# Kernel tuning notes

Hardware: AMD Instinct MI355X
Metric: run time of the kernel (lower is better)

## Reference

```python
import jax, jax.numpy as jnp
import numpy as np

HIDDEN = 64
INPUT = 19


def _lstm_layer(x, Wih, Whh, bih, bhh):
    # x: [B, T, I]; Wih: [4H, I]; Whh: [4H, H]; biases: [4H]
    B, T, _ = x.shape
    H = Whh.shape[1]
    # Input contribution for all timesteps at once (big GEMM).
    zx = jnp.einsum('bti,gi->btg', x, Wih) + bih + bhh  # [B, T, 4H]

    def step(carry, z_t):
        h, c = carry
        z = z_t + h @ Whh.T  # [B, 4H]
        i, f, g, o = jnp.split(z, 4, axis=-1)  # torch gate order: i, f, g, o
        i = jax.nn.sigmoid(i)
        f = jax.nn.sigmoid(f)
        g = jnp.tanh(g)
        o = jax.nn.sigmoid(o)
        c = f * c + i * g
        h = o * jnp.tanh(c)
        return (h, c), h

    h0 = jnp.zeros((B, H), x.dtype)
    (_, _), hs = jax.lax.scan(step, (h0, h0), jnp.swapaxes(zx, 0, 1))
    return jnp.swapaxes(hs, 0, 1)  # [B, T, H]


def setup_inputs() -> dict:
    key = jax.random.key(0)
    ks = jax.random.split(key, 12)
    B, T = 4096, 168
    s = 1.0 / np.sqrt(HIDDEN)  # torch LSTM/Linear init scale
    u = lambda k, shape: jax.random.uniform(k, shape, jnp.float32, -s, s)
    return {
        'x': jax.random.normal(ks[0], (B, T, INPUT), jnp.float32),
        'Wih0': u(ks[1], (4 * HIDDEN, INPUT)),
        'Whh0': u(ks[2], (4 * HIDDEN, HIDDEN)),
        'bih0': u(ks[3], (4 * HIDDEN,)),
        'bhh0': u(ks[4], (4 * HIDDEN,)),
        'Wih1': u(ks[5], (4 * HIDDEN, HIDDEN)),
        'Whh1': u(ks[6], (4 * HIDDEN, HIDDEN)),
        'bih1': u(ks[7], (4 * HIDDEN,)),
        'bhh1': u(ks[8], (4 * HIDDEN,)),
        'Wfc': u(ks[9], (1, HIDDEN)),
        'bfc': u(ks[10], (1,)),
    }


def reference(x, Wih0, Whh0, bih0, bhh0, Wih1, Whh1, bih1, bhh1, Wfc, bfc):
    h1 = _lstm_layer(x, Wih0, Whh0, bih0, bhh0)   # [B, T, H]
    h2 = _lstm_layer(h1, Wih1, Whh1, bih1, bhh1)  # [B, T, H]
    out = h2[:, -1, :] @ Wfc.T + bfc              # [B, 1]
    return out.squeeze(-1)                        # [B]
```

## Files before the change

kernel.cpp:

```cpp
#include <hip/hip_runtime.h>
#include <math.h>

#define T_STEPS 168
#define INP     19
#define HID     64
#define ROWS    16
#define NTH     512
#define HSTH    72
#define XSTH    40

typedef _Float16 half8   __attribute__((ext_vector_type(8)));
typedef float    floatx4 __attribute__((ext_vector_type(4)));

#define KSIG  (-1.4426950408889634f)
#define KTANH ( 2.8853900817779268f)

#if defined(__has_builtin)
#  if __has_builtin(__builtin_amdgcn_exp2f)
#    define EXP2(x) __builtin_amdgcn_exp2f(x)
#  else
#    define EXP2(x) exp2f(x)
#  endif
#else
#  define EXP2(x) exp2f(x)
#endif

__device__ __forceinline__ float sig_pre(float a) {
    return __builtin_amdgcn_rcpf(1.0f + EXP2(a));
}
__device__ __forceinline__ float tanh_pre(float a) {
    return 1.0f - 2.0f * __builtin_amdgcn_rcpf(1.0f + EXP2(a));
}

__global__ __launch_bounds__(NTH) __attribute__((amdgpu_waves_per_eu(2, 2)))
void lstm2_mfma6_kernel(const float* __restrict__ x,
                        const float* __restrict__ Wih0, const float* __restrict__ Whh0,
                        const float* __restrict__ bih0, const float* __restrict__ bhh0,
                        const float* __restrict__ Wih1, const float* __restrict__ Whh1,
                        const float* __restrict__ bih1, const float* __restrict__ bhh1,
                        const float* __restrict__ Wfc,  const float* __restrict__ bfc,
                        float* __restrict__ out)
{
    __shared__ __align__(16) _Float16 xf [2][ROWS][XSTH];
    __shared__ __align__(16) _Float16 h1f[2][ROWS][HSTH];
    __shared__ __align__(16) _Float16 h2f[2][ROWS][HSTH];
    __shared__ float hout[ROWS][HID];

    const int tid  = threadIdx.x;
    const int b0   = blockIdx.x * ROWS;
    const int wv   = tid >> 6;
    const int lane = tid & 63;
    const int quad = lane >> 4;
    const int l16  = lane & 15;
    const int kq   = quad * 8;
    const int lay  = wv >> 2;
    const int uq   = wv & 3;
    const int u    = uq * 16 + l16;

    half8 bfr[4][4];
    float bz[4];
#pragma unroll
    for (int gi = 0; gi < 4; ++gi) {
        const float sc = (gi == 2) ? KTANH : KSIG;
        const int gr = gi * 64 + u;
        if (lay == 0) {
            const float* wr = Wih0 + gr * INP;
#pragma unroll
            for (int e = 0; e < 8; ++e) {
                const int k = kq + e;
                bfr[gi][0][e] = (k < INP) ? (_Float16)(wr[k] * sc) : (_Float16)0.0f;
            }
            const float* hr = Whh0 + gr * HID;
#pragma unroll
            for (int e = 0; e < 8; ++e) {
                bfr[gi][1][e] = (_Float16)(hr[kq + e] * sc);
                bfr[gi][2][e] = (_Float16)(hr[32 + kq + e] * sc);
            }
            bfr[gi][3] = bfr[gi][2];
            bz[gi] = (bih0[gr] + bhh0[gr]) * sc;
        } else {
            const float* ir = Wih1 + gr * HID;
            const float* hr = Whh1 + gr * HID;
#pragma unroll
            for (int e = 0; e < 8; ++e) {
                bfr[gi][0][e] = (_Float16)(ir[kq + e] * sc);
                bfr[gi][1][e] = (_Float16)(ir[32 + kq + e] * sc);
                bfr[gi][2][e] = (_Float16)(hr[kq + e] * sc);
                bfr[gi][3][e] = (_Float16)(hr[32 + kq + e] * sc);
            }
            bz[gi] = (bih1[gr] + bhh1[gr]) * sc;
        }
    }

    float cst[4] = {0.f, 0.f, 0.f, 0.f};

    int srr = 0, sii = 0;
    const float* xsrc = nullptr;
    if (tid < ROWS * INP) {
        srr = tid / INP; sii = tid - srr * INP;
        xsrc = x + ((size_t)(b0 + srr) * T_STEPS) * INP + sii;
    }

    for (int e = tid; e < 2 * ROWS * XSTH; e += NTH) ((_Float16*)xf)[e] = (_Float16)0.f;
    for (int e = tid; e < 2 * ROWS * HSTH; e += NTH) {
        ((_Float16*)h1f)[e] = (_Float16)0.f;
        ((_Float16*)h2f)[e] = (_Float16)0.f;
    }
    __syncthreads();
    float xreg = 0.f;
    if (xsrc) {
        xf[0][srr][sii] = (_Float16)xsrc[0];
        xreg = xsrc[INP];
    }
    __syncthreads();

    for (int t = 0; t <= T_STEPS; ++t) {
        float xnew = 0.f;
        if (xsrc) {
            const int tn = (t + 2 < T_STEPS) ? (t + 2) : (T_STEPS - 1);
            xnew = xsrc[(size_t)tn * INP];
        }
        if (xsrc && (t + 1) < T_STEPS)
            xf[(t + 1) & 1][srr][sii] = (_Float16)xreg;

        const bool act = (lay == 0) ? (t < T_STEPS) : (t >= 1);
        if (act) {
            floatx4 acc[4];
#pragma unroll
            for (int gi = 0; gi < 4; ++gi)
                acc[gi] = (floatx4){bz[gi], bz[gi], bz[gi], bz[gi]};
            if (lay == 0) {
                const half8 ax = *(const half8*)&xf [t & 1][l16][kq];
                const half8 a0 = *(const half8*)&h1f[(t + 1) & 1][l16][kq];
                const half8 a1 = *(const half8*)&h1f[(t + 1) & 1][l16][32 + kq];
#pragma unroll
                for (int gi = 0; gi < 4; ++gi) {
                    acc[gi] = __builtin_amdgcn_mfma_f32_16x16x32_f16(ax, bfr[gi][0], acc[gi], 0, 0, 0);
                    acc[gi] = __builtin_amdgcn_mfma_f32_16x16x32_f16(a0, bfr[gi][1], acc[gi], 0, 0, 0);
                    acc[gi] = __builtin_amdgcn_mfma_f32_16x16x32_f16(a1, bfr[gi][2], acc[gi], 0, 0, 0);
                }
            } else {
                const half8 p0 = *(const half8*)&h1f[(t + 1) & 1][l16][kq];
                const half8 p1 = *(const half8*)&h1f[(t + 1) & 1][l16][32 + kq];
                const half8 q0 = *(const half8*)&h2f[t & 1][l16][kq];
                const half8 q1 = *(const half8*)&h2f[t & 1][l16][32 + kq];
#pragma unroll
                for (int gi = 0; gi < 4; ++gi) {
                    acc[gi] = __builtin_amdgcn_mfma_f32_16x16x32_f16(p0, bfr[gi][0], acc[gi], 0, 0, 0);
                    acc[gi] = __builtin_amdgcn_mfma_f32_16x16x32_f16(p1, bfr[gi][1], acc[gi], 0, 0, 0);
                    acc[gi] = __builtin_amdgcn_mfma_f32_16x16x32_f16(q0, bfr[gi][2], acc[gi], 0, 0, 0);
                    acc[gi] = __builtin_amdgcn_mfma_f32_16x16x32_f16(q1, bfr[gi][3], acc[gi], 0, 0, 0);
                }
            }
#pragma unroll
            for (int rg = 0; rg < 4; ++rg) {
                const float ig = sig_pre (acc[0][rg]);
                const float fg = sig_pre (acc[1][rg]);
                const float gg = tanh_pre(acc[2][rg]);
                const float og = sig_pre (acc[3][rg]);
                cst[rg] = fg * cst[rg] + ig * gg;
                const float hv = og * tanh_pre(KTANH * cst[rg]);
                const int row = quad * 4 + rg;
                if (lay == 0) {
                    h1f[t & 1][row][u] = (_Float16)hv;
                } else {
                    h2f[(t + 1) & 1][row][u] = (_Float16)hv;
                    if (t == T_STEPS) hout[row][u] = hv;
                }
            }
        }
        xreg = xnew;
        __syncthreads();
    }

    if (tid < ROWS) {
        float a = bfc[0];
        const float* hr = hout[tid];
#pragma unroll
        for (int k = 0; k < HID; ++k)
            a = fmaf(hr[k], Wfc[k], a);
        out[b0 + tid] = a;
    }
}

extern "C" void kernel_launch(void* const* d_in, const int* in_sizes, int n_in,
                              void* d_out, int out_size, void* d_ws, size_t ws_size,
                              hipStream_t stream) {
    const float* x    = (const float*)d_in[0];
    const float* Wih0 = (const float*)d_in[1];
    const float* Whh0 = (const float*)d_in[2];
    const float* bih0 = (const float*)d_in[3];
    const float* bhh0 = (const float*)d_in[4];
    const float* Wih1 = (const float*)d_in[5];
    const float* Whh1 = (const float*)d_in[6];
    const float* bih1 = (const float*)d_in[7];
    const float* bhh1 = (const float*)d_in[8];
    const float* Wfc  = (const float*)d_in[9];
    const float* bfc  = (const float*)d_in[10];
    float* out = (float*)d_out;

    const int B = in_sizes[0] / (T_STEPS * INP);
    const int grid = B / ROWS;

    lstm2_mfma6_kernel<<<dim3(grid), dim3(NTH), 0, stream>>>(
        x, Wih0, Whh0, bih0, bhh0, Wih1, Whh1, bih1, bhh1, Wfc, bfc, out);
}
```

Measured before the change: 241.4 us.

## Merge LSTM gate nonlinearities into shared reciprocals and unroll time loop by two

Rewrites the cell update algebraically so that the i, f and g gate activations and the cell update share one combined denominator. The output gate and tanh(c) likewise share a single reciprocal, which cuts the rcp count per element from five to two. The timestep loop is unrolled by two through a macro so double-buffer parities become compile-time constants. The combined products of several (1+exp) terms can overflow for large pre-activations, which risks inf/NaN where the old per-gate form saturated safely; only c is clamped before the final exp.

```diff
diff --git a/kernel.cpp b/kernel.cpp
--- a/kernel.cpp
+++ b/kernel.cpp
@@ -25,15 +25,8 @@
 #  define EXP2(x) exp2f(x)
 #endif
 
-__device__ __forceinline__ float sig_pre(float a) {
-    return __builtin_amdgcn_rcpf(1.0f + EXP2(a));
-}
-__device__ __forceinline__ float tanh_pre(float a) {
-    return 1.0f - 2.0f * __builtin_amdgcn_rcpf(1.0f + EXP2(a));
-}
-
 __global__ __launch_bounds__(NTH) __attribute__((amdgpu_waves_per_eu(2, 2)))
-void lstm2_mfma6_kernel(const float* __restrict__ x,
+void lstm2_mfma8_kernel(const float* __restrict__ x,
                         const float* __restrict__ Wih0, const float* __restrict__ Whh0,
                         const float* __restrict__ bih0, const float* __restrict__ bhh0,
                         const float* __restrict__ Wih1, const float* __restrict__ Whh1,
@@ -92,7 +85,7 @@
         }
     }
 
-    float cst[4] = {0.f, 0.f, 0.f, 0.f};
+    floatx4 cst = (floatx4){0.f, 0.f, 0.f, 0.f};
 
     int srr = 0, sii = 0;
     const float* xsrc = nullptr;
@@ -114,70 +107,113 @@
     }
     __syncthreads();
 
-    for (int t = 0; t <= T_STEPS; ++t) {
-        float xnew = 0.f;
-        if (xsrc) {
-            const int tn = (t + 2 < T_STEPS) ? (t + 2) : (T_STEPS - 1);
-            xnew = xsrc[(size_t)tn * INP];
-        }
-        if (xsrc && (t + 1) < T_STEPS)
-            xf[(t + 1) & 1][srr][sii] = (_Float16)xreg;
-
-        const bool act = (lay == 0) ? (t < T_STEPS) : (t >= 1);
-        if (act) {
-            floatx4 acc[4];
-#pragma unroll
-            for (int gi = 0; gi < 4; ++gi)
-                acc[gi] = (floatx4){bz[gi], bz[gi], bz[gi], bz[gi]};
-            if (lay == 0) {
-                const half8 ax = *(const half8*)&xf [t & 1][l16][kq];
-                const half8 a0 = *(const half8*)&h1f[(t + 1) & 1][l16][kq];
-                const half8 a1 = *(const half8*)&h1f[(t + 1) & 1][l16][32 + kq];
-#pragma unroll
-                for (int gi = 0; gi < 4; ++gi) {
-                    acc[gi] = __builtin_amdgcn_mfma_f32_16x16x32_f16(ax, bfr[gi][0], acc[gi], 0, 0, 0);
-                    acc[gi] = __builtin_amdgcn_mfma_f32_16x16x32_f16(a0, bfr[gi][1], acc[gi], 0, 0, 0);
-                    acc[gi] = __builtin_amdgcn_mfma_f32_16x16x32_f16(a1, bfr[gi][2], acc[gi], 0, 0, 0);
-                }
-            } else {
-                const half8 p0 = *(const half8*)&h1f[(t + 1) & 1][l16][kq];
-                const half8 p1 = *(const half8*)&h1f[(t + 1) & 1][l16][32 + kq];
-                const half8 q0 = *(const half8*)&h2f[t & 1][l16][kq];
-                const half8 q1 = *(const half8*)&h2f[t & 1][l16][32 + kq];
-#pragma unroll
-                for (int gi = 0; gi < 4; ++gi) {
-                    acc[gi] = __builtin_amdgcn_mfma_f32_16x16x32_f16(p0, bfr[gi][0], acc[gi], 0, 0, 0);
-                    acc[gi] = __builtin_amdgcn_mfma_f32_16x16x32_f16(p1, bfr[gi][1], acc[gi], 0, 0, 0);
-                    acc[gi] = __builtin_amdgcn_mfma_f32_16x16x32_f16(q0, bfr[gi][2], acc[gi], 0, 0, 0);
-                    acc[gi] = __builtin_amdgcn_mfma_f32_16x16x32_f16(q1, bfr[gi][3], acc[gi], 0, 0, 0);
-                }
-            }
-#pragma unroll
-            for (int rg = 0; rg < 4; ++rg) {
-                const float ig = sig_pre (acc[0][rg]);
-                const float fg = sig_pre (acc[1][rg]);
-                const float gg = tanh_pre(acc[2][rg]);
-                const float og = sig_pre (acc[3][rg]);
-                cst[rg] = fg * cst[rg] + ig * gg;
-                const float hv = og * tanh_pre(KTANH * cst[rg]);
-                const int row = quad * 4 + rg;
-                if (lay == 0) {
-                    h1f[t & 1][row][u] = (_Float16)hv;
-                } else {
-                    h2f[(t + 1) & 1][row][u] = (_Float16)hv;
-                    if (t == T_STEPS) hout[row][u] = hv;
-                }
-            }
-        }
-        xreg = xnew;
-        __syncthreads();
-    }
+#define STEP(TCUR, PAR, PARX)                                                  \
+    do {                                                                       \
+        float xnew = 0.f;                                                      \
+        if (xsrc) {                                                            \
+            const int tn = ((TCUR) + 2 < T_STEPS) ? ((TCUR) + 2)               \
+                                                  : (T_STEPS - 1);             \
+            xnew = xsrc[(size_t)tn * INP];                                     \
+        }                                                                      \
+        if (xsrc && ((TCUR) + 1) < T_STEPS)                                    \
+            xf[PARX][srr][sii] = (_Float16)xreg;                               \
+        const bool act = (lay == 0) ? ((TCUR) < T_STEPS) : ((TCUR) >= 1);      \
+        if (act) {                                                             \
+            floatx4 acc[4];                                                    \
+            _Pragma("unroll")                                                  \
+            for (int gi = 0; gi < 4; ++gi)                                     \
+                acc[gi] = (floatx4){bz[gi], bz[gi], bz[gi], bz[gi]};           \
+            if (lay == 0) {                                                    \
+                const half8 ax = *(const half8*)&xf [PAR ][l16][kq];           \
+                const half8 a0 = *(const half8*)&h1f[PARX][l16][kq];           \
+                const half8 a1 = *(const half8*)&h1f[PARX][l16][32 + kq];      \
+                _Pragma("unroll")                                              \
+                for (int gi = 0; gi < 4; ++gi) {                               \
+                    acc[gi] = __builtin_amdgcn_mfma_f32_16x16x32_f16(          \
+                        ax, bfr[gi][0], acc[gi], 0, 0, 0);                     \
+                    acc[gi] = __builtin_amdgcn_mfma_f32_16x16x32_f16(          \
+                        a0, bfr[gi][1], acc[gi], 0, 0, 0);                     \
+                    acc[gi] = __builtin_amdgcn_mfma_f32_16x16x32_f16(          \
+                        a1, bfr[gi][2], acc[gi], 0, 0, 0);                     \
+                }                                                              \
+            } else {                                                           \
+                const half8 p0 = *(const half8*)&h1f[PARX][l16][kq];           \
+                const half8 p1 = *(const half8*)&h1f[PARX][l16][32 + kq];      \
+                const half8 q0 = *(const half8*)&h2f[PAR ][l16][kq];           \
+                const half8 q1 = *(const half8*)&h2f[PAR ][l16][32 + kq];      \
+                _Pragma("unroll")                                              \
+                for (int gi = 0; gi < 4; ++gi) {                               \
+                    acc[gi] = __builtin_amdgcn_mfma_f32_16x16x32_f16(          \
+                        p0, bfr[gi][0], acc[gi], 0, 0, 0);                     \
+                    acc[gi] = __builtin_amdgcn_mfma_f32_16x16x32_f16(          \
+                        p1, bfr[gi][1], acc[gi], 0, 0, 0);                     \
+                    acc[gi] = __builtin_amdgcn_mfma_f32_16x16x32_f16(          \
+                        q0, bfr[gi][2], acc[gi], 0, 0, 0);                     \
+                    acc[gi] = __builtin_amdgcn_mfma_f32_16x16x32_f16(          \
+                        q1, bfr[gi][3], acc[gi], 0, 0, 0);                     \
+                }                                                              \
+            }                                                                  \
+              \
+            floatx4 Ai, Af, Eg, Ao;                                            \
+            _Pragma("unroll")                                                  \
+            for (int rg = 0; rg < 4; ++rg) {                                   \
+                Ai[rg] = EXP2(acc[0][rg]);                        \
+                Af[rg] = EXP2(acc[1][rg]);                        \
+                Eg[rg] = EXP2(acc[2][rg]);                       \
+                Ao[rg] = EXP2(acc[3][rg]);                        \
+            }                                                                  \
+            const floatx4 onev = (floatx4){1.f, 1.f, 1.f, 1.f};                \
+            const floatx4 t1 = onev + Af;                                      \
+            const floatx4 t2 = onev + Ai;                                      \
+            const floatx4 t3 = onev + Eg;                                      \
+            const floatx4 t4 = t2 * t3;                                        \
+            const floatx4 num = (Eg - onev) * t1 + cst * t4;                   \
+            const floatx4 den = t1 * t4;                                       \
+            floatx4 rd;                                                        \
+            _Pragma("unroll")                                                  \
+            for (int rg = 0; rg < 4; ++rg)                                     \
+                rd[rg] = __builtin_amdgcn_rcpf(den[rg]);                       \
+            const floatx4 cn = num * rd;                                       \
+            cst = cn;                                                          \
+            floatx4 Ec;                                                        \
+            _Pragma("unroll")                                                  \
+            for (int rg = 0; rg < 4; ++rg) {                                   \
+                const float cc = fminf(fmaxf(cn[rg], -30.0f), 30.0f);          \
+                Ec[rg] = EXP2(KTANH * cc);                       \
+            }                                                                  \
+            const floatx4 dh = (onev + Ao) * (Ec + onev);                      \
+            floatx4 rh;                                                        \
+            _Pragma("unroll")                                                  \
+            for (int rg = 0; rg < 4; ++rg)                                     \
+                rh[rg] = __builtin_amdgcn_rcpf(dh[rg]);                        \
+            const floatx4 hvv = (Ec - onev) * rh;                              \
+            _Pragma("unroll")                                                  \
+            for (int rg = 0; rg < 4; ++rg) {                                   \
+                const int row = quad * 4 + rg;                                 \
+                if (lay == 0) {                                                \
+                    h1f[PAR][row][u] = (_Float16)hvv[rg];           \
+                } else {                                                       \
+                    h2f[PARX][row][u] = (_Float16)hvv[rg];        \
+                    if ((TCUR) == T_STEPS) hout[row][u] = hvv[rg];             \
+                }                                                              \
+            }                                                                  \
+        }                                                                      \
+        xreg = xnew;                \
+        __syncthreads();                          \
+    } while (0)
+
+    for (int t = 0; t < T_STEPS; t += 2) {
+        STEP(t,     0, 1);
+        STEP(t + 1, 1, 0);
+    }
+    STEP(T_STEPS, 0, 1);
+#undef STEP
 
     if (tid < ROWS) {
         float a = bfc[0];
         const float* hr = hout[tid];
 #pragma unroll
-        for (int k = 0; k < HID; ++k)
+    for (int k = 0; k < HID; ++k)
             a = fmaf(hr[k], Wfc[k], a);
         out[b0 + tid] = a;
     }
@@ -202,6 +238,6 @@
     const int B = in_sizes[0] / (T_STEPS * INP);
     const int grid = B / ROWS;
 
-    lstm2_mfma6_kernel<<<dim3(grid), dim3(NTH), 0, stream>>>(
+    lstm2_mfma8_kernel<<<dim3(grid), dim3(NTH), 0, stream>>>(
         x, Wih0, Whh0, bih0, bhh0, Wih1, Whh1, bih1, bhh1, Wfc, bfc, out);
 }
```

After: 248.9 us. 1.03x slower.
